# Kernel tuning notes

Hardware: AMD Instinct MI355X
Metric: run time of the kernel (lower is better)

## Reference

```python
import jax, jax.numpy as jnp
import numpy as np

B, T, D = 8, 2048, 1024

def _ln(x, g, b, eps=1e-5):
    mu = x.mean(-1, keepdims=True)
    var = ((x - mu) ** 2).mean(-1, keepdims=True)
    return (x - mu) * jax.lax.rsqrt(var + eps) * g + b

def setup_inputs() -> dict:
    key = jax.random.key(0)
    ks = jax.random.split(key, 8)
    s = 1.0 / np.sqrt(D)
    return {
        "x": jax.random.normal(ks[0], (B, T, D), jnp.float32),
        "Wq": jax.random.normal(ks[1], (D, D), jnp.float32) * s,
        "bq": jnp.zeros((D,), jnp.float32),
        "Wk": jax.random.normal(ks[2], (D, D), jnp.float32) * s,
        "bk": jnp.zeros((D,), jnp.float32),
        "Wv": jax.random.normal(ks[3], (D, D), jnp.float32) * s,
        "bv": jnp.zeros((D,), jnp.float32),
        "pos_bias": jax.random.normal(ks[4], (T, T), jnp.float32) * 0.1,
        "ln1_g": jnp.ones((D,), jnp.float32),
        "ln1_b": jnp.zeros((D,), jnp.float32),
        "W1": jax.random.normal(ks[5], (D, 4 * D), jnp.float32) * s,
        "b1": jnp.zeros((4 * D,), jnp.float32),
        "W2": jax.random.normal(ks[6], (4 * D, D), jnp.float32) * (1.0 / np.sqrt(4 * D)),
        "b2": jnp.zeros((D,), jnp.float32),
        "ln2_g": jnp.ones((D,), jnp.float32),
        "ln2_b": jnp.zeros((D,), jnp.float32),
    }

def reference(x, Wq, bq, Wk, bk, Wv, bv, pos_bias, ln1_g, ln1_b,
              W1, b1, W2, b2, ln2_g, ln2_b):
    # --- pre-norm AFT-full attention + residual ---
    h = _ln(x, ln1_g, ln1_b)
    q = h @ Wq + bq                      # [B,T,D]
    k = h @ Wk + bk
    v = h @ Wv + bv
    # global-max stabilization (cancels in the ratio)
    ek = jnp.exp(k - jax.lax.stop_gradient(k.max()))
    ew = jnp.exp(pos_bias - jax.lax.stop_gradient(pos_bias.max()))  # [T,T]
    num = jnp.einsum('ts,bsd->btd', ew, ek * v)
    den = jnp.einsum('ts,bsd->btd', ew, ek)
    attn = jax.nn.sigmoid(q) * (num / den)
    x = attn + x
    # --- pre-norm MLP + residual ---
    h = _ln(x, ln2_g, ln2_b)
    h = jax.nn.relu(h @ W1 + b1) @ W2 + b2
    return h + x
```

## Files before the change

kernel.cpp:

```cpp
#include <hip/hip_runtime.h>
#include <hip/hip_bf16.h>
#include <stdint.h>

typedef __hip_bfloat16 bf16;
typedef __attribute__((ext_vector_type(4))) float f32x4;
typedef __attribute__((ext_vector_type(8))) short bf16x8;

#define BB   8
#define TT   2048
#define DD   1024
#define MM   (BB * TT)

enum { EPI_Q = 0, EPI_KV, EPI_ND, EPI_MLP1, EPI_MLP2 };

static __device__ __forceinline__ void async_ld16(const bf16* g, bf16* l) {
  __builtin_amdgcn_global_load_lds(
      (const __attribute__((address_space(1))) void*)g,
      (__attribute__((address_space(3))) void*)l, 16, 0, 0);
}

template<int EPI>
__global__ __launch_bounds__(512, 2)
void gemm_bt(const bf16* __restrict__ A, const bf16* __restrict__ B,
             int M, int N, int K,
             long long strideAz, long long strideBz,
             float* __restrict__ Cf,
             bf16* __restrict__ Cb, long long strideCz,
             const float* __restrict__ bias,
             const float* __restrict__ add,
             bf16* __restrict__ ekv)
{
  (void)M;
  __shared__ __align__(16) bf16 lds[65536];

  const int tid  = threadIdx.x;
  const int wave = tid >> 6;
  const int lane = tid & 63;

  const int nwg = (int)gridDim.x;
  const int bid = (int)blockIdx.x;
  const int swz = (bid & 7) * (nwg >> 3) + (bid >> 3);
  int bn, bm, bz;
  if constexpr (EPI == EPI_ND) {
    bn = swz & 7; bm = (swz >> 3) & 7; bz = swz >> 6;
  } else {
    const int nbn = N >> 8;
    const int lnb = 31 - __clz(nbn);
    bn = swz & (nbn - 1); bm = swz >> lnb; bz = 0;
  }
  A += (size_t)bz * strideAz;
  B += (size_t)bz * strideBz;

  const int wm = (wave >> 2) * 128;
  const int wn = (wave & 3) * 64;

  const int lr = lane >> 2;
  const int lc = (((lane & 3) ^ ((lane >> 3) & 3))) * 8;
  const bf16* Ag0 = A + ((size_t)bm * 256 + wave * 32 + lr) * K + lc;
  const bf16* Bg0 = B + ((size_t)bn * 256 + wave * 32 + lr) * K + lc;
  const size_t K16 = (size_t)16 * K;
  const int ldsAW = wave * 1024;
  const int ldsBW = 32768 + wave * 1024;
  const int NT = K >> 5;

  auto stageA = [&](int tt) {
    const int bo = (tt & 3) * 8192;
    const bf16* g = Ag0 + (size_t)(tt & (NT - 1)) * 32;
    async_ld16(g,       &lds[bo + ldsAW]);
    async_ld16(g + K16, &lds[bo + ldsAW + 512]);
  };
  auto stageB = [&](int tt) {
    const int bo = (tt & 3) * 8192;
    const bf16* g = Bg0 + (size_t)(tt & (NT - 1)) * 32;
    async_ld16(g,       &lds[bo + ldsBW]);
    async_ld16(g + K16, &lds[bo + ldsBW + 512]);
  };

  f32x4 acc[8][4];
#pragma unroll
  for (int i = 0; i < 8; ++i)
#pragma unroll
    for (int j = 0; j < 4; ++j) acc[i][j] = {0.f, 0.f, 0.f, 0.f};

  stageA(0); stageB(0);
  stageA(1); stageB(1);
  stageA(2); stageB(2);
  __builtin_amdgcn_sched_barrier(0);
  asm volatile("s_waitcnt vmcnt(8)" ::: "memory");
  __builtin_amdgcn_s_barrier();
  __builtin_amdgcn_sched_barrier(0);

  const int fm32 = (lane & 15) * 32;
  const int qs = (((lane >> 4) ^ ((lane >> 1) & 3))) * 8;

  bf16x8 bfrP[4], bfrN[4], afA[4], afB[4];

  {
    const int ab0 = wm * 32 + fm32 + qs;
    const int bb0 = 32768 + wn * 32 + fm32 + qs;
#pragma unroll
    for (int j = 0; j < 4; ++j) bfrP[j] = *(const bf16x8*)&lds[bb0 + j * 512];
#pragma unroll
    for (int i = 0; i < 4; ++i) afA[i] = *(const bf16x8*)&lds[ab0 + i * 512];
  }
  __builtin_amdgcn_sched_barrier(0);

#define TILE_BODY(t, bfrC, bfrX)                                               \
  {                                                                            \
    const int ab  = ((t) & 3) * 8192 + wm * 32 + fm32 + qs;                    \
    const int abn = (((t) + 1) & 3) * 8192 + wm * 32 + fm32 + qs;              \
    const int bbn = 32768 + (((t) + 1) & 3) * 8192 + wn * 32 + fm32 + qs;      \
                                                        \
    _Pragma("unroll")                                                          \
    for (int i = 0; i < 4; ++i)                                                \
      afB[i] = *(const bf16x8*)&lds[ab + 2048 + i * 512];                      \
    stageA((t) + 3);                                                           \
    __builtin_amdgcn_sched_barrier(0);                                         \
    asm volatile("s_waitcnt vmcnt(6) lgkmcnt(4)" ::: "memory");                \
    __builtin_amdgcn_sched_barrier(0);                                         \
    __builtin_amdgcn_s_setprio(1);                                             \
    _Pragma("unroll")                                                          \
    for (int i = 0; i < 4; ++i)                                                \
      _Pragma("unroll")                                                        \
      for (int j = 0; j < 4; ++j)                                              \
        acc[i][j] = __builtin_amdgcn_mfma_f32_16x16x32_bf16(                   \
            afA[i], bfrC[j], acc[i][j], 0, 0, 0);                              \
    __builtin_amdgcn_s_setprio(0);                                             \
    __builtin_amdgcn_s_barrier();                                              \
    __builtin_amdgcn_sched_barrier(0);                                         \
                                                        \
    _Pragma("unroll")                                                          \
    for (int j = 0; j < 4; ++j)                                                \
      bfrX[j] = *(const bf16x8*)&lds[bbn + j * 512];                           \
    _Pragma("unroll")                                                          \
    for (int i = 0; i < 4; ++i)                                                \
      afA[i] = *(const bf16x8*)&lds[abn + i * 512];                            \
    stageB((t) + 3);                                                           \
    __builtin_amdgcn_sched_barrier(0);                                         \
    asm volatile("s_waitcnt lgkmcnt(8)" ::: "memory");                         \
    __builtin_amdgcn_sched_barrier(0);                                         \
    __builtin_amdgcn_s_setprio(1);                                             \
    _Pragma("unroll")                                                          \
    for (int i = 0; i < 4; ++i)                                                \
      _Pragma("unroll")                                                        \
      for (int j = 0; j < 4; ++j)                                              \
        acc[4 + i][j] = __builtin_amdgcn_mfma_f32_16x16x32_bf16(               \
            afB[i], bfrC[j], acc[4 + i][j], 0, 0, 0);                          \
    __builtin_amdgcn_s_setprio(0);                                             \
    __builtin_amdgcn_s_barrier();                                              \
    __builtin_amdgcn_sched_barrier(0);                                         \
  }

  for (int tp = 0; tp < NT; tp += 2) {
    TILE_BODY(tp,     bfrP, bfrN);
    TILE_BODY(tp + 1, bfrN, bfrP);
  }
#undef TILE_BODY

  const int cr = (lane >> 4) * 4;
  const int cc = lane & 15;
#pragma unroll
  for (int i = 0; i < 8; ++i) {
#pragma unroll
    for (int j = 0; j < 4; ++j) {
#pragma unroll
      for (int r = 0; r < 4; ++r) {
        const int gm = bm * 256 + wm + i * 16 + cr + r;
        const int gn = bn * 256 + wn + j * 16 + cc;
        float v = acc[i][j][r];
        if constexpr (EPI == EPI_Q) {
          v += bias[gn];
          Cb[(size_t)gm * N + gn] = __float2bfloat16(v);
        } else if constexpr (EPI == EPI_KV) {
          if ((r & 1) == 0) {
            const int d = gm >> 1;
            const float ek = __expf(acc[i][j][r] + bias[d]);
            const float vv = acc[i][j][r + 1] + add[d];
            const int b = gn >> 11, t = gn & (TT - 1);
            const size_t base = ((size_t)b << 22);
            ekv[base + (size_t)(1024 + d) * TT + t] = __float2bfloat16(ek);
            ekv[base + (size_t)d * TT + t] = __float2bfloat16(ek * vv);
          }
        } else if constexpr (EPI == EPI_ND) {
          Cb[(size_t)bz * strideCz + (size_t)gm * N + gn] =
              __float2bfloat16(v);
        } else if constexpr (EPI == EPI_MLP1) {
          v = fmaxf(v + bias[gn], 0.0f);
          Cb[(size_t)gm * N + gn] = __float2bfloat16(v);
        } else {
          v += bias[gn] + add[(size_t)gm * N + gn];
          Cf[(size_t)gm * N + gn] = v;
        }
      }
    }
  }
}

__global__ __launch_bounds__(256)
void transpose_cast(const float* __restrict__ W, bf16* __restrict__ Wt,
                    int K, int N, int rs, int ro)
{
  __shared__ float tile[32][33];
  const int n0 = blockIdx.x * 32, k0 = blockIdx.y * 32;
  const int tx = threadIdx.x, ty = threadIdx.y;
#pragma unroll
  for (int i = 0; i < 32; i += 8)
    tile[ty + i][tx] = W[(size_t)(k0 + ty + i) * N + n0 + tx];
  __syncthreads();
#pragma unroll
  for (int i = 0; i < 32; i += 8)
    Wt[((size_t)(n0 + ty + i) * rs + ro) * K + k0 + tx] =
        __float2bfloat16(tile[tx][ty + i]);
}

__global__ __launch_bounds__(256)
void transpose3(const float* __restrict__ Wq, const float* __restrict__ Wk,
                const float* __restrict__ Wv, bf16* __restrict__ wqt,
                bf16* __restrict__ wkv)
{
  __shared__ float tile[32][33];
  const int z = blockIdx.z;
  const float* W = (z == 0) ? Wq : (z == 1) ? Wk : Wv;
  bf16* Wt = (z == 0) ? wqt : wkv;
  const int rs = (z == 0) ? 1 : 2;
  const int ro = (z == 2) ? 1 : 0;
  const int n0 = blockIdx.x * 32, k0 = blockIdx.y * 32;
  const int tx = threadIdx.x, ty = threadIdx.y;
#pragma unroll
  for (int i = 0; i < 32; i += 8)
    tile[ty + i][tx] = W[(size_t)(k0 + ty + i) * DD + n0 + tx];
  __syncthreads();
#pragma unroll
  for (int i = 0; i < 32; i += 8)
    Wt[((size_t)(n0 + ty + i) * rs + ro) * DD + k0 + tx] =
        __float2bfloat16(tile[tx][ty + i]);
}

__global__ __launch_bounds__(256)
void ln_ew_kernel(const float* __restrict__ x, const float* __restrict__ g,
                  const float* __restrict__ b, bf16* __restrict__ out,
                  const float* __restrict__ pb, bf16* __restrict__ ew)
{
  const int blk = blockIdx.x;
  const int tid = threadIdx.x;
  if (blk >= MM) {
    const size_t gid = (size_t)(blk - MM) * 256 + tid;
    const float4 v = *(const float4*)(pb + gid * 4);
    union { bf16 h[4]; unsigned long long u; } pk;
    pk.h[0] = __float2bfloat16(__expf(v.x));
    pk.h[1] = __float2bfloat16(__expf(v.y));
    pk.h[2] = __float2bfloat16(__expf(v.z));
    pk.h[3] = __float2bfloat16(__expf(v.w));
    *(unsigned long long*)(ew + gid * 4) = pk.u;
    return;
  }
  const int row = blk;
  const float4 v = ((const float4*)(x + (size_t)row * DD))[tid];
  float s  = v.x + v.y + v.z + v.w;
  float s2 = v.x * v.x + v.y * v.y + v.z * v.z + v.w * v.w;
#pragma unroll
  for (int o = 32; o; o >>= 1) {
    s  += __shfl_down(s, o);
    s2 += __shfl_down(s2, o);
  }
  __shared__ float red[8];
  if ((tid & 63) == 0) { red[tid >> 6] = s; red[4 + (tid >> 6)] = s2; }
  __syncthreads();
  const float ts  = red[0] + red[1] + red[2] + red[3];
  const float ts2 = red[4] + red[5] + red[6] + red[7];
  const float mu = ts * (1.0f / DD);
  const float rs = rsqrtf(ts2 * (1.0f / DD) - mu * mu + 1e-5f);
  const float4 gv = ((const float4*)g)[tid];
  const float4 bv = ((const float4*)b)[tid];
  union { bf16 h[4]; unsigned long long u; } pk;
  pk.h[0] = __float2bfloat16((v.x - mu) * rs * gv.x + bv.x);
  pk.h[1] = __float2bfloat16((v.y - mu) * rs * gv.y + bv.y);
  pk.h[2] = __float2bfloat16((v.z - mu) * rs * gv.z + bv.z);
  pk.h[3] = __float2bfloat16((v.w - mu) * rs * gv.w + bv.w);
  ((unsigned long long*)(out + (size_t)row * DD))[tid] = pk.u;
}

__global__ __launch_bounds__(256)
void combine_ln_kernel(const bf16* __restrict__ q, const bf16* __restrict__ nd,
                       const float* __restrict__ x,
                       const float* __restrict__ g, const float* __restrict__ b,
                       float* __restrict__ x2, bf16* __restrict__ hout)
{
  const int row = blockIdx.x;
  const int tid = threadIdx.x;
  const int c = tid * 4;
  const bf16* ndr = nd + (size_t)row * 2048;
  union { unsigned long long u; bf16 h[4]; } un, ud, uq;
  un.u = *(const unsigned long long*)(ndr + c);
  ud.u = *(const unsigned long long*)(ndr + 1024 + c);
  uq.u = *(const unsigned long long*)(q + (size_t)row * DD + c);
  const float4 xv = *(const float4*)(x + (size_t)row * DD + c);
  float4 o;
  o.x = xv.x + (__bfloat162float(un.h[0]) / __bfloat162float(ud.h[0])) /
                   (1.0f + __expf(-__bfloat162float(uq.h[0])));
  o.y = xv.y + (__bfloat162float(un.h[1]) / __bfloat162float(ud.h[1])) /
                   (1.0f + __expf(-__bfloat162float(uq.h[1])));
  o.z = xv.z + (__bfloat162float(un.h[2]) / __bfloat162float(ud.h[2])) /
                   (1.0f + __expf(-__bfloat162float(uq.h[2])));
  o.w = xv.w + (__bfloat162float(un.h[3]) / __bfloat162float(ud.h[3])) /
                   (1.0f + __expf(-__bfloat162float(uq.h[3])));
  *(float4*)(x2 + (size_t)row * DD + c) = o;

  float s  = o.x + o.y + o.z + o.w;
  float s2 = o.x * o.x + o.y * o.y + o.z * o.z + o.w * o.w;
#pragma unroll
  for (int off = 32; off; off >>= 1) {
    s  += __shfl_down(s, off);
    s2 += __shfl_down(s2, off);
  }
  __shared__ float red[8];
  if ((tid & 63) == 0) { red[tid >> 6] = s; red[4 + (tid >> 6)] = s2; }
  __syncthreads();
  const float ts  = red[0] + red[1] + red[2] + red[3];
  const float ts2 = red[4] + red[5] + red[6] + red[7];
  const float mu = ts * (1.0f / DD);
  const float rs = rsqrtf(ts2 * (1.0f / DD) - mu * mu + 1e-5f);
  const float4 gv = ((const float4*)g)[tid];
  const float4 bv = ((const float4*)b)[tid];
  union { bf16 h[4]; unsigned long long u; } pk;
  pk.h[0] = __float2bfloat16((o.x - mu) * rs * gv.x + bv.x);
  pk.h[1] = __float2bfloat16((o.y - mu) * rs * gv.y + bv.y);
  pk.h[2] = __float2bfloat16((o.z - mu) * rs * gv.z + bv.z);
  pk.h[3] = __float2bfloat16((o.w - mu) * rs * gv.w + bv.w);
  ((unsigned long long*)(hout + (size_t)row * DD))[tid] = pk.u;
}

extern "C" void kernel_launch(void* const* d_in, const int* in_sizes, int n_in,
                              void* d_out, int out_size, void* d_ws,
                              size_t ws_size, hipStream_t stream)
{
  (void)in_sizes; (void)n_in; (void)out_size; (void)ws_size;
  const float* x   = (const float*)d_in[0];
  const float* Wq  = (const float*)d_in[1];
  const float* bq  = (const float*)d_in[2];
  const float* Wk  = (const float*)d_in[3];
  const float* bk  = (const float*)d_in[4];
  const float* Wv  = (const float*)d_in[5];
  const float* bv  = (const float*)d_in[6];
  const float* pb  = (const float*)d_in[7];
  const float* g1  = (const float*)d_in[8];
  const float* be1 = (const float*)d_in[9];
  const float* W1  = (const float*)d_in[10];
  const float* bm1 = (const float*)d_in[11];
  const float* W2  = (const float*)d_in[12];
  const float* bm2 = (const float*)d_in[13];
  const float* g2  = (const float*)d_in[14];
  const float* be2 = (const float*)d_in[15];
  float* out = (float*)d_out;

  const size_t MiB = 1024 * 1024;
  char* w = (char*)d_ws;
  bf16* hbf = (bf16*)w;  w += (size_t)MM * DD * 2;
  bf16* wqt = (bf16*)w;  w += (size_t)DD * DD * 2;
  bf16* wkv = (bf16*)w;  w += (size_t)2 * DD * DD * 2;
  bf16* w1t = (bf16*)w;  w += (size_t)4096 * DD * 2;
  bf16* w2t = (bf16*)w;  w += (size_t)DD * 4096 * 2;
  char* scr = w;
  bf16* qbf = (bf16*)scr;
  bf16* ewb = (bf16*)(scr + 32 * MiB);
  bf16* ekv = (bf16*)(scr + 40 * MiB);
  bf16* nd  = (bf16*)(scr + 104 * MiB);
  bf16* mid = (bf16*)scr;
  float* x2 = out;

  const dim3 tb(32, 8);
  transpose3<<<dim3(DD / 32, DD / 32, 3), tb, 0, stream>>>(Wq, Wk, Wv,
                                                           wqt, wkv);
  transpose_cast<<<dim3(4096 / 32, DD / 32), tb, 0, stream>>>(
      W1, w1t, DD, 4096, 1, 0);
  transpose_cast<<<dim3(DD / 32, 4096 / 32), tb, 0, stream>>>(
      W2, w2t, 4096, DD, 1, 0);

  ln_ew_kernel<<<MM + (TT * TT / 4) / 256, 256, 0, stream>>>(
      x, g1, be1, hbf, pb, ewb);

  gemm_bt<EPI_Q><<<(MM / 256) * (DD / 256), 512, 0, stream>>>(
      hbf, wqt, MM, DD, DD, 0, 0, nullptr, qbf, 0, bq, nullptr, nullptr);
  gemm_bt<EPI_KV><<<(2048 / 256) * (MM / 256), 512, 0, stream>>>(
      wkv, hbf, 2048, MM, DD, 0, 0, nullptr, nullptr, 0, bk, bv, ekv);
  gemm_bt<EPI_ND><<<BB * (TT / 256) * (TT / 256), 512, 0, stream>>>(
      ewb, ekv, TT, TT, TT, 0, (long long)TT * TT, nullptr, nd,
      (long long)TT * TT, nullptr, nullptr, nullptr);

  combine_ln_kernel<<<MM, 256, 0, stream>>>(qbf, nd, x, g2, be2, x2, hbf);

  gemm_bt<EPI_MLP1><<<(MM / 256) * (4096 / 256), 512, 0, stream>>>(
      hbf, w1t, MM, 4096, DD, 0, 0, nullptr, mid, 0, bm1, nullptr, nullptr);
  gemm_bt<EPI_MLP2><<<(MM / 256) * (DD / 256), 512, 0, stream>>>(
      mid, w2t, MM, DD, 4096, 0, 0, out, nullptr, 0, bm2, x2, nullptr);
}
```

Baseline: 705.6 us.

## Load B fragments directly from global into registers, halve LDS footprint

Result: slower. 991.5 us (+40.5%).

```diff
diff --git a/kernel.cpp b/kernel.cpp
--- a/kernel.cpp
+++ b/kernel.cpp
@@ -31,7 +31,7 @@
              bf16* __restrict__ ekv)
 {
   (void)M;
-  __shared__ __align__(16) bf16 lds[65536];
+  __shared__ __align__(16) bf16 lds[32768];
 
   const int tid  = threadIdx.x;
   const int wave = tid >> 6;
@@ -57,10 +57,8 @@
   const int lr = lane >> 2;
   const int lc = (((lane & 3) ^ ((lane >> 3) & 3))) * 8;
   const bf16* Ag0 = A + ((size_t)bm * 256 + wave * 32 + lr) * K + lc;
-  const bf16* Bg0 = B + ((size_t)bn * 256 + wave * 32 + lr) * K + lc;
   const size_t K16 = (size_t)16 * K;
   const int ldsAW = wave * 1024;
-  const int ldsBW = 32768 + wave * 1024;
   const int NT = K >> 5;
 
   auto stageA = [&](int tt) {
@@ -69,12 +67,10 @@
     async_ld16(g,       &lds[bo + ldsAW]);
     async_ld16(g + K16, &lds[bo + ldsAW + 512]);
   };
-  auto stageB = [&](int tt) {
-    const int bo = (tt & 3) * 8192;
-    const bf16* g = Bg0 + (size_t)(tt & (NT - 1)) * 32;
-    async_ld16(g,       &lds[bo + ldsBW]);
-    async_ld16(g + K16, &lds[bo + ldsBW + 512]);
-  };
+
+  const int fm = lane & 15;
+  const int q4 = lane >> 4;
+  const bf16* Bfg = B + ((size_t)bn * 256 + wn + fm) * K + q4 * 8;
 
   f32x4 acc[8][4];
 #pragma unroll
@@ -82,41 +78,36 @@
 #pragma unroll
     for (int j = 0; j < 4; ++j) acc[i][j] = {0.f, 0.f, 0.f, 0.f};
 
-  stageA(0); stageB(0);
-  stageA(1); stageB(1);
-  stageA(2); stageB(2);
+  bf16x8 bfP[4], bfN[4], af[4];
+
+  {
+    const bf16* p = Bfg;
+#pragma unroll
+    for (int j = 0; j < 4; ++j) bfP[j] = *(const bf16x8*)(p + j * K16);
+  }
+  stageA(0); stageA(1); stageA(2);
   __builtin_amdgcn_sched_barrier(0);
-  asm volatile("s_waitcnt vmcnt(8)" ::: "memory");
+  asm volatile("s_waitcnt vmcnt(0)" ::: "memory");
   __builtin_amdgcn_s_barrier();
   __builtin_amdgcn_sched_barrier(0);
 
   const int fm32 = (lane & 15) * 32;
   const int qs = (((lane >> 4) ^ ((lane >> 1) & 3))) * 8;
 
-  bf16x8 bfrP[4], bfrN[4], afA[4], afB[4];
-
-  {
-    const int ab0 = wm * 32 + fm32 + qs;
-    const int bb0 = 32768 + wn * 32 + fm32 + qs;
-#pragma unroll
-    for (int j = 0; j < 4; ++j) bfrP[j] = *(const bf16x8*)&lds[bb0 + j * 512];
-#pragma unroll
-    for (int i = 0; i < 4; ++i) afA[i] = *(const bf16x8*)&lds[ab0 + i * 512];
-  }
-  __builtin_amdgcn_sched_barrier(0);
-
-#define TILE_BODY(t, bfrC, bfrX)                                               \
+#define TILE_BODY(t, bfC, bfX)                                                 \
   {                                                                            \
-    const int ab  = ((t) & 3) * 8192 + wm * 32 + fm32 + qs;                    \
-    const int abn = (((t) + 1) & 3) * 8192 + wm * 32 + fm32 + qs;              \
-    const int bbn = 32768 + (((t) + 1) & 3) * 8192 + wn * 32 + fm32 + qs;      \
-                                                        \
+    const int ab = ((t) & 3) * 8192 + wm * 32 + fm32 + qs;                     \
+                                       \
+    {                                                                          \
+      const bf16* p = Bfg + (size_t)(((t) + 1) & (NT - 1)) * 32;               \
+      _Pragma("unroll")                                                        \
+      for (int j = 0; j < 4; ++j) bfX[j] = *(const bf16x8*)(p + j * K16);      \
+    }                                                                          \
+    stageA((t) + 3);                                                           \
     _Pragma("unroll")                                                          \
-    for (int i = 0; i < 4; ++i)                                                \
-      afB[i] = *(const bf16x8*)&lds[ab + 2048 + i * 512];                      \
-    stageA((t) + 3);                                                           \
-    __builtin_amdgcn_sched_barrier(0);                                         \
-    asm volatile("s_waitcnt vmcnt(6) lgkmcnt(4)" ::: "memory");                \
+    for (int i = 0; i < 4; ++i) af[i] = *(const bf16x8*)&lds[ab + i * 512];    \
+    __builtin_amdgcn_sched_barrier(0);                                         \
+    asm volatile("s_waitcnt vmcnt(8) lgkmcnt(0)" ::: "memory");                \
     __builtin_amdgcn_sched_barrier(0);                                         \
     __builtin_amdgcn_s_setprio(1);                                             \
     _Pragma("unroll")                                                          \
@@ -124,20 +115,14 @@
       _Pragma("unroll")                                                        \
       for (int j = 0; j < 4; ++j)                                              \
         acc[i][j] = __builtin_amdgcn_mfma_f32_16x16x32_bf16(                   \
-            afA[i], bfrC[j], acc[i][j], 0, 0, 0);                              \
+            af[i], bfC[j], acc[i][j], 0, 0, 0);                                \
     __builtin_amdgcn_s_setprio(0);                                             \
-    __builtin_amdgcn_s_barrier();                                              \
-    __builtin_amdgcn_sched_barrier(0);                                         \
-                                                        \
-    _Pragma("unroll")                                                          \
-    for (int j = 0; j < 4; ++j)                                                \
-      bfrX[j] = *(const bf16x8*)&lds[bbn + j * 512];                           \
+    __builtin_amdgcn_sched_barrier(0);                                         \
     _Pragma("unroll")                                                          \
     for (int i = 0; i < 4; ++i)                                                \
-      afA[i] = *(const bf16x8*)&lds[abn + i * 512];                            \
-    stageB((t) + 3);                                                           \
-    __builtin_amdgcn_sched_barrier(0);                                         \
-    asm volatile("s_waitcnt lgkmcnt(8)" ::: "memory");                         \
+      af[i] = *(const bf16x8*)&lds[ab + 2048 + i * 512];                       \
+    __builtin_amdgcn_sched_barrier(0);                                         \
+    asm volatile("s_waitcnt lgkmcnt(0)" ::: "memory");                         \
     __builtin_amdgcn_sched_barrier(0);                                         \
     __builtin_amdgcn_s_setprio(1);                                             \
     _Pragma("unroll")                                                          \
@@ -145,15 +130,16 @@
       _Pragma("unroll")                                                        \
       for (int j = 0; j < 4; ++j)                                              \
         acc[4 + i][j] = __builtin_amdgcn_mfma_f32_16x16x32_bf16(               \
-            afB[i], bfrC[j], acc[4 + i][j], 0, 0, 0);                          \
+            af[i], bfC[j], acc[4 + i][j], 0, 0, 0);                            \
     __builtin_amdgcn_s_setprio(0);                                             \
+    __builtin_amdgcn_sched_barrier(0);                                         \
     __builtin_amdgcn_s_barrier();                                              \
     __builtin_amdgcn_sched_barrier(0);                                         \
   }
 
   for (int tp = 0; tp < NT; tp += 2) {
-    TILE_BODY(tp,     bfrP, bfrN);
-    TILE_BODY(tp + 1, bfrN, bfrP);
+    TILE_BODY(tp,     bfP, bfN);
+    TILE_BODY(tp + 1, bfN, bfP);
   }
 #undef TILE_BODY
 
```
